# Performance work log

Measured on AMD Instinct MI355X. Metric: run time of the kernel, lower is better.

## Reference

```python
import jax, jax.numpy as jnp
import numpy as np

B, T, N, D = 16, 24, 512, 128
Z, OUT_DIM = 12, 1
NEG_SLOPE = 0.01

def setup_inputs() -> dict:
    key = jax.random.key(0)
    ks = jax.random.split(key, 7)
    H_temp = jax.random.normal(ks[0], (B, T, N, D), dtype=jnp.float32)
    H_spatial = jax.random.normal(ks[1], (B, T, N, D), dtype=jnp.float32)
    H_sem = jax.random.normal(ks[2], (B, T, N, D), dtype=jnp.float32)
    # Conv1d(3D -> D, k=1) folded to a matrix; torch-like init scale
    s1 = 1.0 / np.sqrt(3 * D)
    s2 = 1.0 / np.sqrt(D)
    W1 = jax.random.uniform(ks[3], (D, 3 * D), jnp.float32, -s1, s1)
    b1 = jax.random.uniform(ks[4], (D,), jnp.float32, -s1, s1)
    W2 = jax.random.uniform(ks[5], (Z * OUT_DIM, D), jnp.float32, -s2, s2)
    b2 = jax.random.uniform(ks[6], (Z * OUT_DIM,), jnp.float32, -s2, s2)
    return {"H_temp": H_temp, "H_spatial": H_spatial, "H_sem": H_sem,
            "W1": W1, "b1": b1, "W2": W2, "b2": b2}

def reference(H_temp, H_spatial, H_sem, W1, b1, W2, b2):
    # kernel_size=1 convs are per-timestep linear maps, and only the last
    # timestep survives the final slice, so slice first (bit-identical math).
    fused_last = jnp.concatenate(
        [H_temp[:, -1], H_spatial[:, -1], H_sem[:, -1]], axis=-1)  # [B,N,3D]
    y = jnp.einsum('bnc,dc->bnd', fused_last, W1) + b1              # [B,N,D]
    y = jnp.where(y > 0, y, NEG_SLOPE * y)                          # LeakyReLU
    y = jnp.einsum('bnd,zd->bnz', y, W2) + b2                       # [B,N,Z*OUT]
    y = y.reshape(B, N, Z, OUT_DIM).transpose(0, 2, 1, 3)           # [B,Z,N,OUT]
    return y
```

## Files before the change

### kernel.cpp

```cpp
#include <hip/hip_runtime.h>
#include <hip/hip_bf16.h>

typedef short  short8  __attribute__((ext_vector_type(8)));
typedef float  floatx4 __attribute__((ext_vector_type(4)));

#define B_  16
#define T_  24
#define N_  512
#define D_  128
#define Z_  12

#define LSTRIDE 136

__device__ __forceinline__ short bf16_bits(float x) {
    __hip_bfloat16 h = __float2bfloat16(x);
    return *reinterpret_cast<short*>(&h);
}

__device__ __forceinline__ short8 pack8(const float* s) {
    short8 v;
    #pragma unroll
    for (int i = 0; i < 4; ++i) v[i] = bf16_bits(s[i]);
    #pragma unroll
    for (int i = 0; i < 4; ++i) v[4 + i] = bf16_bits(s[4 + i]);
    return v;
}

__global__ __launch_bounds__(256, 2) void fused_out_kernel(
    const void* __restrict__ Ht_v,
    const void* __restrict__ Hs_v,
    const void* __restrict__ Hm_v,
    const void* __restrict__ W1_v,
    const void* __restrict__ b1_v,
    const void* __restrict__ W2_v,
    const void* __restrict__ b2_v,
    void* __restrict__ out_v)
{
    __shared__ __attribute__((aligned(16))) short lw1[128 * LSTRIDE];
    __shared__ __attribute__((aligned(16))) short la [32  * LSTRIDE];
    __shared__ __attribute__((aligned(16))) short ly [32  * LSTRIDE];
    __shared__ __attribute__((aligned(16))) short lw2[16  * LSTRIDE];
    __shared__ float lb1[128];
    __shared__ float lb2[16];

    bool fm;
    {
        const unsigned short* p = (const unsigned short*)W1_v;
        int big = 0;
        #pragma unroll
        for (int i = 0; i < 64; ++i) {
            unsigned e = (p[i] >> 7) & 0xFF;
            big += (e >= 134);
        }
        fm = (big > 0);
    }

    const int tid  = threadIdx.x;
    const int lane = tid & 63;
    const int w    = tid >> 6;
    const int quad = lane >> 4;
    const int l16  = lane & 15;

    {
        int z  = tid >> 4;
        int c8 = (tid & 15) * 8;
        short8 v = {};
        if (z < Z_) {
            if (fm) v = pack8((const float*)W2_v + z * 128 + c8);
            else    v = *(const short8*)((const short*)W2_v + z * 128 + c8);
        }
        *(short8*)&lw2[z * LSTRIDE + c8] = v;
        if (tid < 128)
            lb1[tid] = fm ? ((const float*)b1_v)[tid]
                          : __bfloat162float(((const __hip_bfloat16*)b1_v)[tid]);
        if (tid < 16)
            lb2[tid] = (tid < Z_)
                       ? (fm ? ((const float*)b2_v)[tid]
                             : __bfloat162float(((const __hip_bfloat16*)b2_v)[tid]))
                       : 0.0f;
    }

    const int r0 = (w & 1) * 16;
    const int n0 = (w >> 1) * 64;
    const int rowbase = blockIdx.x * 32;

    floatx4 acc[4];
    #pragma unroll
    for (int t = 0; t < 4; ++t) acc[t] = (floatx4){0.f, 0.f, 0.f, 0.f};

    for (int kc = 0; kc < 3; ++kc) {
        __syncthreads();

        #pragma unroll
        for (int it = 0; it < 8; ++it) {
            int q  = tid + it * 256;
            int d  = q >> 4;
            int c8 = (q & 15) * 8;
            short8 v;
            if (fm) v = pack8((const float*)W1_v + d * 384 + kc * 128 + c8);
            else    v = *(const short8*)((const short*)W1_v + d * 384 + kc * 128 + c8);
            *(short8*)&lw1[d * LSTRIDE + c8] = v;
        }
        const void* H = (kc == 0) ? Ht_v : (kc == 1) ? Hs_v : Hm_v;
        #pragma unroll
        for (int it = 0; it < 2; ++it) {
            int q  = tid + it * 256;
            int r  = q >> 4;
            int c8 = (q & 15) * 8;
            int grow = rowbase + r;
            int bb = grow >> 9, nn = grow & 511;
            int off = ((bb * T_ + (T_ - 1)) * N_ + nn) * D_ + c8;
            short8 v;
            if (fm) v = pack8((const float*)H + off);
            else    v = *(const short8*)((const short*)H + off);
            *(short8*)&la[r * LSTRIDE + c8] = v;
        }
        __syncthreads();

        #pragma unroll
        for (int ks = 0; ks < 4; ++ks) {
            int ko = ks * 32 + quad * 8;
            short8 af = *(const short8*)&la[(r0 + l16) * LSTRIDE + ko];
            #pragma unroll
            for (int t = 0; t < 4; ++t) {
                short8 bf = *(const short8*)&lw1[(n0 + t * 16 + l16) * LSTRIDE + ko];
                acc[t] = __builtin_amdgcn_mfma_f32_16x16x32_bf16(af, bf, acc[t], 0, 0, 0);
            }
        }
    }

    #pragma unroll
    for (int t = 0; t < 4; ++t) {
        int col = n0 + t * 16 + l16;
        float bias = lb1[col];
        #pragma unroll
        for (int r = 0; r < 4; ++r) {
            float v = acc[t][r] + bias;
            v = (v > 0.f) ? v : 0.01f * v;
            int row = r0 + quad * 4 + r;
            ly[row * LSTRIDE + col] = bf16_bits(v);
        }
    }

    __syncthreads();

    if (w < 2) {
        int rr0 = w * 16;
        floatx4 acc2 = (floatx4){0.f, 0.f, 0.f, 0.f};
        #pragma unroll
        for (int ks = 0; ks < 4; ++ks) {
            int ko = ks * 32 + quad * 8;
            short8 af = *(const short8*)&ly [(rr0 + l16) * LSTRIDE + ko];
            short8 bf = *(const short8*)&lw2[ l16        * LSTRIDE + ko];
            acc2 = __builtin_amdgcn_mfma_f32_16x16x32_bf16(af, bf, acc2, 0, 0, 0);
        }
        int z = l16;
        if (z < Z_) {
            float bias = lb2[z];
            #pragma unroll
            for (int r = 0; r < 4; ++r) {
                int grow = rowbase + rr0 + quad * 4 + r;
                int bb = grow >> 9, nn = grow & 511;
                float v = acc2[r] + bias;
                int idx = (bb * Z_ + z) * N_ + nn;
                if (fm) ((float*)out_v)[idx] = v;
                else    ((__hip_bfloat16*)out_v)[idx] = __float2bfloat16(v);
            }
        }
    }
}

extern "C" void kernel_launch(void* const* d_in, const int* in_sizes, int n_in,
                              void* d_out, int out_size, void* d_ws, size_t ws_size,
                              hipStream_t stream) {
    (void)in_sizes; (void)n_in; (void)d_ws; (void)ws_size; (void)out_size;
    fused_out_kernel<<<256, 256, 0, stream>>>(
        d_in[0],
        d_in[1],
        d_in[2],
        d_in[3],
        d_in[4],
        d_in[5],
        d_in[6],
        d_out);
}
```

Before: 228.3 us.

## Load MFMA fragments directly from global memory, drop LDS staging, halve rows per block

Removes the LDS staging of W1, activations and W2. Each wave now loads its MFMA A/B fragments straight from global memory with vectorized float4 loads and converts them to bf16 in registers, which eliminates the per-chunk barriers. Blocks now handle 16 rows instead of 32, doubling the grid to 512 blocks, and the output is written with vectorized stores. In exchange, W1 is read from global memory (or L2) by every wave of every block with no shared reuse, which raises cache traffic.

```diff
diff --git a/kernel.cpp b/kernel.cpp
--- a/kernel.cpp
+++ b/kernel.cpp
@@ -2,6 +2,7 @@
 #include <hip/hip_bf16.h>
 
 typedef short  short8  __attribute__((ext_vector_type(8)));
+typedef short  short4v __attribute__((ext_vector_type(4)));
 typedef float  floatx4 __attribute__((ext_vector_type(4)));
 
 #define B_  16
@@ -17,13 +18,23 @@
     return *reinterpret_cast<short*>(&h);
 }
 
-__device__ __forceinline__ short8 pack8(const float* s) {
+__device__ __forceinline__ short8 cvt8(floatx4 a, floatx4 b) {
     short8 v;
     #pragma unroll
-    for (int i = 0; i < 4; ++i) v[i] = bf16_bits(s[i]);
+    for (int i = 0; i < 4; ++i) v[i] = bf16_bits(a[i]);
     #pragma unroll
-    for (int i = 0; i < 4; ++i) v[4 + i] = bf16_bits(s[4 + i]);
+    for (int i = 0; i < 4; ++i) v[4 + i] = bf16_bits(b[i]);
     return v;
+}
+
+__device__ __forceinline__ short8 load_frag(const void* p, int off, bool fm) {
+    if (fm) {
+        const float* f = (const float*)p + off;
+        floatx4 a = *(const floatx4*)f;
+        floatx4 b = *(const floatx4*)(f + 4);
+        return cvt8(a, b);
+    }
+    return *(const short8*)((const short*)p + off);
 }
 
 __global__ __launch_bounds__(256, 2) void fused_out_kernel(
@@ -36,22 +47,15 @@
     const void* __restrict__ b2_v,
     void* __restrict__ out_v)
 {
-    __shared__ __attribute__((aligned(16))) short lw1[128 * LSTRIDE];
-    __shared__ __attribute__((aligned(16))) short la [32  * LSTRIDE];
-    __shared__ __attribute__((aligned(16))) short ly [32  * LSTRIDE];
-    __shared__ __attribute__((aligned(16))) short lw2[16  * LSTRIDE];
+    __shared__ __attribute__((aligned(16))) short ly[16 * LSTRIDE];
     __shared__ float lb1[128];
-    __shared__ float lb2[16];
 
     bool fm;
     {
         const unsigned short* p = (const unsigned short*)W1_v;
         int big = 0;
         #pragma unroll
-        for (int i = 0; i < 64; ++i) {
-            unsigned e = (p[i] >> 7) & 0xFF;
-            big += (e >= 134);
-        }
+        for (int i = 0; i < 64; ++i) big += (((p[i] >> 7) & 0xFF) >= 134);
         fm = (big > 0);
     }
 
@@ -61,110 +65,71 @@
     const int quad = lane >> 4;
     const int l16  = lane & 15;
 
-    {
-        int z  = tid >> 4;
-        int c8 = (tid & 15) * 8;
-        short8 v = {};
-        if (z < Z_) {
-            if (fm) v = pack8((const float*)W2_v + z * 128 + c8);
-            else    v = *(const short8*)((const short*)W2_v + z * 128 + c8);
-        }
-        *(short8*)&lw2[z * LSTRIDE + c8] = v;
-        if (tid < 128)
-            lb1[tid] = fm ? ((const float*)b1_v)[tid]
-                          : __bfloat162float(((const __hip_bfloat16*)b1_v)[tid]);
-        if (tid < 16)
-            lb2[tid] = (tid < Z_)
-                       ? (fm ? ((const float*)b2_v)[tid]
-                             : __bfloat162float(((const __hip_bfloat16*)b2_v)[tid]))
-                       : 0.0f;
-    }
+    if (tid < 128)
+        lb1[tid] = fm ? ((const float*)b1_v)[tid]
+                      : __bfloat162float(((const __hip_bfloat16*)b1_v)[tid]);
 
-    const int r0 = (w & 1) * 16;
-    const int n0 = (w >> 1) * 64;
-    const int rowbase = blockIdx.x * 32;
+    const int rowbase = blockIdx.x * 16;
+    const int bb  = rowbase >> 9;
+    const int nn0 = rowbase & 511;
+    const int abase = ((bb * T_ + (T_ - 1)) * N_ + (nn0 + l16)) * D_;
 
-    floatx4 acc[4];
+    floatx4 acc[2];
+    acc[0] = (floatx4){0.f, 0.f, 0.f, 0.f};
+    acc[1] = (floatx4){0.f, 0.f, 0.f, 0.f};
+
     #pragma unroll
-    for (int t = 0; t < 4; ++t) acc[t] = (floatx4){0.f, 0.f, 0.f, 0.f};
-
-    for (int kc = 0; kc < 3; ++kc) {
-        __syncthreads();
-
+    for (int ks = 0; ks < 12; ++ks) {
+        const void* H = (ks < 4) ? Ht_v : (ks < 8) ? Hs_v : Hm_v;
+        const int ka = (ks & 3) * 32 + quad * 8;
+        short8 af = load_frag(H, abase + ka, fm);
         #pragma unroll
-        for (int it = 0; it < 8; ++it) {
-            int q  = tid + it * 256;
-            int d  = q >> 4;
-            int c8 = (q & 15) * 8;
-            short8 v;
-            if (fm) v = pack8((const float*)W1_v + d * 384 + kc * 128 + c8);
-            else    v = *(const short8*)((const short*)W1_v + d * 384 + kc * 128 + c8);
-            *(short8*)&lw1[d * LSTRIDE + c8] = v;
-        }
-        const void* H = (kc == 0) ? Ht_v : (kc == 1) ? Hs_v : Hm_v;
-        #pragma unroll
-        for (int it = 0; it < 2; ++it) {
-            int q  = tid + it * 256;
-            int r  = q >> 4;
-            int c8 = (q & 15) * 8;
-            int grow = rowbase + r;
-            int bb = grow >> 9, nn = grow & 511;
-            int off = ((bb * T_ + (T_ - 1)) * N_ + nn) * D_ + c8;
-            short8 v;
-            if (fm) v = pack8((const float*)H + off);
-            else    v = *(const short8*)((const short*)H + off);
-            *(short8*)&la[r * LSTRIDE + c8] = v;
-        }
-        __syncthreads();
-
-        #pragma unroll
-        for (int ks = 0; ks < 4; ++ks) {
-            int ko = ks * 32 + quad * 8;
-            short8 af = *(const short8*)&la[(r0 + l16) * LSTRIDE + ko];
-            #pragma unroll
-            for (int t = 0; t < 4; ++t) {
-                short8 bf = *(const short8*)&lw1[(n0 + t * 16 + l16) * LSTRIDE + ko];
-                acc[t] = __builtin_amdgcn_mfma_f32_16x16x32_bf16(af, bf, acc[t], 0, 0, 0);
-            }
+        for (int t = 0; t < 2; ++t) {
+            const int col = w * 32 + t * 16 + l16;
+            short8 bf = load_frag(W1_v, col * 384 + ks * 32 + quad * 8, fm);
+            acc[t] = __builtin_amdgcn_mfma_f32_16x16x32_bf16(af, bf, acc[t], 0, 0, 0);
         }
     }
 
     #pragma unroll
-    for (int t = 0; t < 4; ++t) {
-        int col = n0 + t * 16 + l16;
-        float bias = lb1[col];
+    for (int t = 0; t < 2; ++t) {
+        const int col = w * 32 + t * 16 + l16;
+        const float bias = lb1[col];
         #pragma unroll
         for (int r = 0; r < 4; ++r) {
             float v = acc[t][r] + bias;
             v = (v > 0.f) ? v : 0.01f * v;
-            int row = r0 + quad * 4 + r;
-            ly[row * LSTRIDE + col] = bf16_bits(v);
+            ly[(quad * 4 + r) * LSTRIDE + col] = bf16_bits(v);
         }
     }
 
     __syncthreads();
 
-    if (w < 2) {
-        int rr0 = w * 16;
+    if (w == 0) {
         floatx4 acc2 = (floatx4){0.f, 0.f, 0.f, 0.f};
+        const int z = l16;
         #pragma unroll
         for (int ks = 0; ks < 4; ++ks) {
-            int ko = ks * 32 + quad * 8;
-            short8 af = *(const short8*)&ly [(rr0 + l16) * LSTRIDE + ko];
-            short8 bf = *(const short8*)&lw2[ l16        * LSTRIDE + ko];
+            const int ko = ks * 32 + quad * 8;
+            short8 af = *(const short8*)&ly[l16 * LSTRIDE + ko];
+            short8 bf = (z < Z_) ? load_frag(W2_v, z * 128 + ko, fm)
+                                 : (short8){};
             acc2 = __builtin_amdgcn_mfma_f32_16x16x32_bf16(af, bf, acc2, 0, 0, 0);
         }
-        int z = l16;
         if (z < Z_) {
-            float bias = lb2[z];
-            #pragma unroll
-            for (int r = 0; r < 4; ++r) {
-                int grow = rowbase + rr0 + quad * 4 + r;
-                int bb = grow >> 9, nn = grow & 511;
-                float v = acc2[r] + bias;
-                int idx = (bb * Z_ + z) * N_ + nn;
-                if (fm) ((float*)out_v)[idx] = v;
-                else    ((__hip_bfloat16*)out_v)[idx] = __float2bfloat16(v);
+            const float bias = fm ? ((const float*)b2_v)[z]
+                                  : __bfloat162float(((const __hip_bfloat16*)b2_v)[z]);
+            const int nbase = (bb * Z_ + z) * N_ + nn0 + quad * 4;
+            if (fm) {
+                floatx4 o;
+                #pragma unroll
+                for (int r = 0; r < 4; ++r) o[r] = acc2[r] + bias;
+                *(floatx4*)((float*)out_v + nbase) = o;
+            } else {
+                short4v o;
+                #pragma unroll
+                for (int r = 0; r < 4; ++r) o[r] = bf16_bits(acc2[r] + bias);
+                *(short4v*)((short*)out_v + nbase) = o;
             }
         }
     }
@@ -174,13 +139,6 @@
                               void* d_out, int out_size, void* d_ws, size_t ws_size,
                               hipStream_t stream) {
     (void)in_sizes; (void)n_in; (void)d_ws; (void)ws_size; (void)out_size;
-    fused_out_kernel<<<256, 256, 0, stream>>>(
-        d_in[0],
-        d_in[1],
-        d_in[2],
-        d_in[3],
-        d_in[4],
-        d_in[5],
-        d_in[6],
-        d_out);
+    fused_out_kernel<<<512, 256, 0, stream>>>(
+        d_in[0], d_in[1], d_in[2], d_in[3], d_in[4], d_in[5], d_in[6], d_out);
 }
```

Result: no change. 230.1 us (+0.8%).
